# Optimization experiments

Hardware: AMD Instinct MI355X
Metric: run time of the kernel (lower is better)

The kernel has to match this reference:

```python
import jax, jax.numpy as jnp
import numpy as np

T, B, I, H, C, O = 4096, 8, 256, 512, 1024, 512
SCHEDULE = 1.0
UPPER_T = 0.3
NIND = int((1.0 - SCHEDULE) * (C - 2) * UPPER_T) + 1  # = 1 (argmax WTA)


def setup_inputs() -> dict:
    key = jax.random.key(0)
    ks = jax.random.split(key, 8)
    def lin(k, fan_out, fan_in):
        s = 1.0 / np.sqrt(fan_in)
        kw, kb = jax.random.split(k)
        return (jax.random.uniform(kw, (fan_out, fan_in), jnp.float32, -s, s),
                jax.random.uniform(kb, (fan_out,), jnp.float32, -s, s))
    i2m_w, i2m_b = lin(ks[0], H, I)
    m2h_w, m2h_b = lin(ks[1], C, H)
    h2o_w, h2o_b = lin(ks[2], O, C)
    return {
        "x": jax.random.normal(ks[3], (T, B, I), jnp.float32),
        "hidden1": jnp.zeros((1,), jnp.float32),  # unused dummy (overwritten in torch forward)
        "i2m_w": i2m_w, "i2m_b": i2m_b,
        "m2h_w": m2h_w, "m2h_b": m2h_b,
        "h2o_w": h2o_w, "h2o_b": h2o_b,
    }


def reference(x, hidden1, i2m_w, i2m_b, m2h_w, m2h_b, h2o_w, h2o_b):
    # linear -> relu
    h = jax.nn.relu(jnp.einsum('tbi,hi->tbh', x, i2m_w) + i2m_b)
    # linear -> relu -> concept pre-activations [T,B,C]
    c = jax.nn.relu(jnp.einsum('tbh,ch->tbc', h, m2h_w) + m2h_b)
    # winner-take-all: top-Nind scatter mask (replaces CPU argsort round-trip)
    _, idx = jax.lax.top_k(c, NIND)  # [T,B,NIND]
    t_ix = jnp.arange(c.shape[0])[:, None, None]
    b_ix = jnp.arange(c.shape[1])[None, :, None]
    mask = jnp.zeros_like(c).at[t_ix, b_ix, idx].set(1.0)
    m = c * mask
    # L2 normalize over concept axis
    m = m / jnp.linalg.norm(m, axis=-1, keepdims=True)
    out = jnp.einsum('tbc,oc->tbo', m, h2o_w) + h2o_b
    return jax.nn.log_softmax(out, axis=-1)
```

## Files before the change

### kernel.cpp

```cpp
#include <hip/hip_runtime.h>
#include <stdint.h>

#define M_ROWS 32768
#define I_DIM 256
#define H_DIM 512
#define C_DIM 1024
#define O_DIM 512

typedef __attribute__((ext_vector_type(8))) short bf16x8;
typedef __attribute__((ext_vector_type(4))) float f32x4;

__device__ __forceinline__ ushort bf16_rne(float f) {
    unsigned u = __float_as_uint(f);
    unsigned r = u + 0x7FFFu + ((u >> 16) & 1u);
    return (ushort)(r >> 16);
}
__device__ __forceinline__ float bf16_f32(ushort h) {
    return __uint_as_float(((unsigned)h) << 16);
}
__device__ __forceinline__ void split2(float f, ushort& hi, ushort& mid) {
    hi = bf16_rne(f);
    mid = bf16_rne(f - bf16_f32(hi));
}

__device__ __forceinline__ void async_ld16(const void* g, void* l) {
    __builtin_amdgcn_global_load_lds(
        (const __attribute__((address_space(1))) void*)g,
        (__attribute__((address_space(3))) void*)l, 16, 0, 0);
}

__device__ __forceinline__ unsigned long long packvi(float v, int col) {
    unsigned u = __float_as_uint(v);
    u = (u & 0x80000000u) ? ~u : (u | 0x80000000u);
    return ((unsigned long long)u << 32) | (unsigned)(~col);
}

__device__ __forceinline__ int slot_of(int kc, int row) {
    return (kc + ((row >> 1) & 3)) & 3;
}

__global__ __launch_bounds__(256)
void prep(const float* __restrict__ W1, ushort* __restrict__ w1h, ushort* __restrict__ w1m,
          const float* __restrict__ W2, ushort* __restrict__ w2h, ushort* __restrict__ w2m,
          const float* __restrict__ Wo, const float* __restrict__ bo,
          float* __restrict__ LS, unsigned long long* __restrict__ part) {
    __shared__ float sred[4];
    const int b = blockIdx.x;
    const int t = threadIdx.x;
    if (b < 320) {
        const int isW1 = (b < 64);
        const float* W = isW1 ? W1 : W2;
        ushort* hh = isW1 ? w1h : w2h;
        ushort* mm = isW1 ? w1m : w2m;
        const int K = isW1 ? I_DIM : H_DIM;
        const int cpr = K >> 3;
        int gid = (isW1 ? b : b - 64) * 256 + t;
        int row = gid / cpr;
        int rem = gid - row * cpr;
        int g = rem >> 2, kc = rem & 3;
        float4 v0 = *(const float4*)(W + (size_t)gid * 8);
        float4 v1 = *(const float4*)(W + (size_t)gid * 8 + 4);
        __align__(16) ushort h[8], m[8];
        float f[8];
        *(float4*)&f[0] = v0; *(float4*)&f[4] = v1;
        #pragma unroll
        for (int j = 0; j < 8; ++j) split2(f[j], h[j], m[j]);
        size_t dst = (size_t)row * K + g * 32 + slot_of(kc, row) * 8;
        *(uint4*)(hh + dst) = *(uint4*)h;
        *(uint4*)(mm + dst) = *(uint4*)m;
    } else if (b < 1344) {
        const int j = b - 320;
        float l0 = Wo[(size_t)t * C_DIM + j] + bo[t];
        float l1 = Wo[(size_t)(t + 256) * C_DIM + j] + bo[t + 256];

        float mx = fmaxf(l0, l1);
        #pragma unroll
        for (int off = 1; off < 64; off <<= 1)
            mx = fmaxf(mx, __shfl_xor(mx, off, 64));
        if ((t & 63) == 0) sred[t >> 6] = mx;
        __syncthreads();
        mx = fmaxf(fmaxf(sred[0], sred[1]), fmaxf(sred[2], sred[3]));
        __syncthreads();

        float s = expf(l0 - mx) + expf(l1 - mx);
        #pragma unroll
        for (int off = 1; off < 64; off <<= 1)
            s += __shfl_xor(s, off, 64);
        if ((t & 63) == 0) sred[t >> 6] = s;
        __syncthreads();
        s = sred[0] + sred[1] + sred[2] + sred[3];

        float lse = mx + logf(s);
        LS[(size_t)j * O_DIM + t] = l0 - lse;
        LS[(size_t)j * O_DIM + t + 256] = l1 - lse;
    } else {
        part[(b - 1344) * 256 + t] = 0ull;
    }
}

__global__ __launch_bounds__(256, 4)
void gemm1_mfma(const float* __restrict__ X, const ushort* __restrict__ W1h,
                const ushort* __restrict__ W1m, const float* __restrict__ b1,
                ushort* __restrict__ Hh, ushort* __restrict__ Hm) {
    __shared__ __align__(16) ushort LB[16384];
    ushort* As0 = LB;
    ushort* As1 = LB + 4096;
    ushort* Bs0 = LB + 8192;
    ushort* Bs1 = LB + 12288;

    const int tid = threadIdx.x;
    const int lane = tid & 63, wave = tid >> 6;
    const int wm = wave >> 1, wn = wave & 1;
    const int lcol = lane & 15, quad = lane >> 4;
    const int mBase = blockIdx.x * 128;
    const int nBase = blockIdx.y * 128;
    const int s_row = tid >> 1, s_half = tid & 1;
    const int bplane = wave >> 1;
    const ushort* wp = bplane ? W1m : W1h;
    const int brow0 = (wave & 1) * 64;
    const int lrow = lane >> 2, lk = (lane & 3) * 8;

    f32x4 acc[4][4];
    #pragma unroll
    for (int i = 0; i < 4; ++i)
        #pragma unroll
        for (int j = 0; j < 4; ++j)
            acc[i][j] = (f32x4){0.f, 0.f, 0.f, 0.f};

    int aoff[4], boff[4];
    #pragma unroll
    for (int t = 0; t < 4; ++t) {
        int ra = wm * 64 + t * 16 + lcol;
        int rb = wn * 64 + t * 16 + lcol;
        aoff[t] = ra * 32 + slot_of(quad, ra) * 8;
        boff[t] = rb * 32 + slot_of(quad, rb) * 8;
    }
    const int sl0 = slot_of(s_half * 2,     s_row);
    const int sl1 = slot_of(s_half * 2 + 1, s_row);

    for (int ks = 0; ks < I_DIM / 32; ++ks) {
        const int k0 = ks * 32;
        const float* ap = X + (size_t)(mBase + s_row) * I_DIM + k0 + s_half * 16;
        float4 f0 = ((const float4*)ap)[0];
        float4 f1 = ((const float4*)ap)[1];
        float4 f2 = ((const float4*)ap)[2];
        float4 f3 = ((const float4*)ap)[3];

        __syncthreads();

        #pragma unroll
        for (int i = 0; i < 4; ++i) {
            int r = brow0 + i * 16;
            const ushort* g = wp + (size_t)(nBase + r + lrow) * I_DIM + k0 + lk;
            async_ld16(g, (bplane ? Bs1 : Bs0) + r * 32);
        }

        float f[16];
        *(float4*)&f[0] = f0; *(float4*)&f[4] = f1;
        *(float4*)&f[8] = f2; *(float4*)&f[12] = f3;
        bf16x8 h0, h1, m0, m1;
        #pragma unroll
        for (int j = 0; j < 8; ++j) {
            ushort hu, mu;
            split2(f[j], hu, mu);
            h0[j] = (short)hu; m0[j] = (short)mu;
            split2(f[j + 8], hu, mu);
            h1[j] = (short)hu; m1[j] = (short)mu;
        }
        *(bf16x8*)&As0[s_row * 32 + sl0 * 8] = h0;
        *(bf16x8*)&As0[s_row * 32 + sl1 * 8] = h1;
        *(bf16x8*)&As1[s_row * 32 + sl0 * 8] = m0;
        *(bf16x8*)&As1[s_row * 32 + sl1 * 8] = m1;

        __syncthreads();

        bf16x8 af[4][2];
        #pragma unroll
        for (int mt = 0; mt < 4; ++mt) {
            af[mt][0] = *(const bf16x8*)&As0[aoff[mt]];
            af[mt][1] = *(const bf16x8*)&As1[aoff[mt]];
        }
        #pragma unroll
        for (int nt = 0; nt < 4; ++nt) {
            bf16x8 bh = *(const bf16x8*)&Bs0[boff[nt]];
            bf16x8 bm = *(const bf16x8*)&Bs1[boff[nt]];
            #pragma unroll
            for (int mt = 0; mt < 4; ++mt) {
                f32x4 a = acc[mt][nt];
                a = __builtin_amdgcn_mfma_f32_16x16x32_bf16(af[mt][1], bh, a, 0, 0, 0);
                a = __builtin_amdgcn_mfma_f32_16x16x32_bf16(af[mt][0], bm, a, 0, 0, 0);
                a = __builtin_amdgcn_mfma_f32_16x16x32_bf16(af[mt][0], bh, a, 0, 0, 0);
                acc[mt][nt] = a;
            }
        }
    }

    #pragma unroll
    for (int plane = 0; plane < 2; ++plane) {
        __syncthreads();
        #pragma unroll
        for (int nt = 0; nt < 4; ++nt) {
            int colRel = wn * 64 + nt * 16 + lcol;
            int g = colRel >> 5, kc = (colRel >> 3) & 3, pos = colRel & 7;
            float bias = b1[nBase + colRel];
            #pragma unroll
            for (int mt = 0; mt < 4; ++mt) {
                #pragma unroll
                for (int r = 0; r < 4; ++r) {
                    int rowRel = wm * 64 + mt * 16 + quad * 4 + r;
                    float v = fmaxf(acc[mt][nt][r] + bias, 0.f);
                    ushort hu, mu;
                    split2(v, hu, mu);
                    LB[rowRel * 128 + g * 32 + slot_of(kc, rowRel) * 8 + pos]
                        = plane ? mu : hu;
                }
            }
        }
        __syncthreads();
        ushort* dstp = plane ? Hm : Hh;
        #pragma unroll
        for (int l = 0; l < 8; ++l) {
            int c = l * 256 + tid;
            int row = c >> 4, idx = c & 15;
            *(uint4*)(dstp + (size_t)(mBase + row) * H_DIM + nBase + idx * 8)
                = *(const uint4*)&LB[row * 128 + idx * 8];
        }
    }
}

__global__ __launch_bounds__(256, 4)
void gemm2_mfma(const ushort* __restrict__ Hh, const ushort* __restrict__ Hm,
                const ushort* __restrict__ W2h, const ushort* __restrict__ W2m,
                const float* __restrict__ b2,
                unsigned long long* __restrict__ part) {
    __shared__ __align__(16) ushort As[2][128 * 32];
    __shared__ __align__(16) ushort Bs[2][128 * 32];
    const int tid = threadIdx.x;
    const int lane = tid & 63, wave = tid >> 6;
    const int wm = wave >> 1, wn = wave & 1;
    const int lcol = lane & 15, quad = lane >> 4;
    const int mBase = blockIdx.x * 128;
    const int nBase = blockIdx.y * 128;
    const int lrow = lane >> 2, lk = (lane & 3) * 8;

    const ushort* gsrc;
    ushort* lbase;
    switch (wave) {
        case 0: gsrc = Hh  + (size_t)mBase * H_DIM; lbase = As[0]; break;
        case 1: gsrc = Hm  + (size_t)mBase * H_DIM; lbase = As[1]; break;
        case 2: gsrc = W2h + (size_t)nBase * H_DIM; lbase = Bs[0]; break;
        default: gsrc = W2m + (size_t)nBase * H_DIM; lbase = Bs[1]; break;
    }

    f32x4 acc[4][4];
    #pragma unroll
    for (int i = 0; i < 4; ++i)
        #pragma unroll
        for (int j = 0; j < 4; ++j)
            acc[i][j] = (f32x4){0.f, 0.f, 0.f, 0.f};

    int aoff[4], boff[4];
    #pragma unroll
    for (int t = 0; t < 4; ++t) {
        int ra = wm * 64 + t * 16 + lcol;
        int rb = wn * 64 + t * 16 + lcol;
        aoff[t] = ra * 32 + slot_of(quad, ra) * 8;
        boff[t] = rb * 32 + slot_of(quad, rb) * 8;
    }

    for (int ks = 0; ks < H_DIM / 32; ++ks) {
        const int k0 = ks * 32;
        __syncthreads();
        #pragma unroll
        for (int j = 0; j < 8; ++j) {
            const ushort* g = gsrc + (size_t)(j * 16 + lrow) * H_DIM + k0 + lk;
            async_ld16(g, lbase + j * 512);
        }
        __syncthreads();

        bf16x8 af[4][2];
        #pragma unroll
        for (int mt = 0; mt < 4; ++mt) {
            af[mt][0] = *(const bf16x8*)&As[0][aoff[mt]];
            af[mt][1] = *(const bf16x8*)&As[1][aoff[mt]];
        }
        #pragma unroll
        for (int nt = 0; nt < 4; ++nt) {
            bf16x8 bh = *(const bf16x8*)&Bs[0][boff[nt]];
            bf16x8 bm = *(const bf16x8*)&Bs[1][boff[nt]];
            #pragma unroll
            for (int mt = 0; mt < 4; ++mt) {
                f32x4 a = acc[mt][nt];
                a = __builtin_amdgcn_mfma_f32_16x16x32_bf16(af[mt][1], bh, a, 0, 0, 0);
                a = __builtin_amdgcn_mfma_f32_16x16x32_bf16(af[mt][0], bm, a, 0, 0, 0);
                a = __builtin_amdgcn_mfma_f32_16x16x32_bf16(af[mt][0], bh, a, 0, 0, 0);
                acc[mt][nt] = a;
            }
        }
    }

    #pragma unroll
    for (int mt = 0; mt < 4; ++mt) {
        #pragma unroll
        for (int r = 0; r < 4; ++r) {
            unsigned long long best = 0ull;
            #pragma unroll
            for (int nt = 0; nt < 4; ++nt) {
                int col = nBase + wn * 64 + nt * 16 + lcol;
                float v = acc[mt][nt][r] + b2[col];
                unsigned long long p = packvi(v, col);
                if (p > best) best = p;
            }
            #pragma unroll
            for (int off = 1; off < 16; off <<= 1) {
                unsigned long long o = __shfl_xor((long long)best, off, 64);
                if (o > best) best = o;
            }
            if (lcol == 0) {
                int row = mBase + wm * 64 + mt * 16 + quad * 4 + r;
                atomicMax(&part[row], best);
            }
        }
    }
}

__global__ __launch_bounds__(256)
void gather_out(const unsigned long long* __restrict__ part,
                const float* __restrict__ LS, float* __restrict__ out) {
    const int tid = threadIdx.x;
    const int row = blockIdx.x * 2 + (tid >> 7);
    const int q = tid & 127;
    unsigned long long best = part[row];
    unsigned u = (unsigned)(best >> 32);
    float v = (u & 0x80000000u) ? __uint_as_float(u ^ 0x80000000u)
                                : __uint_as_float(~u);
    int col = (int)(~(unsigned)best) & (C_DIM - 1);
    int j = (v > 0.f) ? col : 0;
    float4 val = ((const float4*)LS)[(size_t)j * 128 + q];
    ((float4*)out)[(size_t)row * 128 + q] = val;
}

extern "C" void kernel_launch(void* const* d_in, const int* in_sizes, int n_in,
                              void* d_out, int out_size, void* d_ws, size_t ws_size,
                              hipStream_t stream) {
    const float* x     = (const float*)d_in[0];
    const float* i2m_w = (const float*)d_in[2];
    const float* i2m_b = (const float*)d_in[3];
    const float* m2h_w = (const float*)d_in[4];
    const float* m2h_b = (const float*)d_in[5];
    const float* h2o_w = (const float*)d_in[6];
    const float* h2o_b = (const float*)d_in[7];
    float* out = (float*)d_out;

    char* ws = (char*)d_ws;
    ushort* w1h = (ushort*)(ws);
    ushort* w1m = (ushort*)(ws + 262144);
    ushort* w2h = (ushort*)(ws + 524288);
    ushort* w2m = (ushort*)(ws + 1572864);
    float*  LS  = (float*)(ws + 2621440);
    unsigned long long* part = (unsigned long long*)(ws + 4718592);

    ushort* Hh = (ushort*)d_out;
    ushort* Hm = Hh + (size_t)M_ROWS * H_DIM;

    prep<<<1472, 256, 0, stream>>>(i2m_w, w1h, w1m, m2h_w, w2h, w2m,
                                   h2o_w, h2o_b, LS, part);
    gemm1_mfma<<<dim3(M_ROWS / 128, H_DIM / 128), 256, 0, stream>>>(
        x, w1h, w1m, i2m_b, Hh, Hm);
    gemm2_mfma<<<dim3(M_ROWS / 128, C_DIM / 128), 256, 0, stream>>>(
        Hh, Hm, w2h, w2m, m2h_b, part);
    gather_out<<<M_ROWS / 2, 256, 0, stream>>>(part, LS, out);
}
```

Baseline: 258.8 us.

## Double-buffer LDS staging in both GEMMs with tile swizzle and MFMA priority

Both GEMM kernels now use two LDS buffers. The next K-slice's global loads (async for the weights and H, register-staged for X) are issued before the current slice's MFMAs, and each iteration drops to a single barrier. Block indices are remapped so that neighbouring blocks share M/N tiles, for better L2 reuse. s_setprio raises wave priority around the MFMA section. The price is double the LDS footprint, with launch bounds lowered to 2 blocks per CU, which reduces occupancy.

```diff
diff --git a/kernel.cpp b/kernel.cpp
--- a/kernel.cpp
+++ b/kernel.cpp
@@ -98,22 +98,22 @@
     }
 }
 
-__global__ __launch_bounds__(256, 4)
+__global__ __launch_bounds__(256, 2)
 void gemm1_mfma(const float* __restrict__ X, const ushort* __restrict__ W1h,
                 const ushort* __restrict__ W1m, const float* __restrict__ b1,
                 ushort* __restrict__ Hh, ushort* __restrict__ Hm) {
-    __shared__ __align__(16) ushort LB[16384];
-    ushort* As0 = LB;
-    ushort* As1 = LB + 4096;
-    ushort* Bs0 = LB + 8192;
-    ushort* Bs1 = LB + 12288;
+    __shared__ __align__(16) ushort As[2][2][4096];
+    __shared__ __align__(16) ushort Bs[2][2][4096];
 
     const int tid = threadIdx.x;
     const int lane = tid & 63, wave = tid >> 6;
     const int wm = wave >> 1, wn = wave & 1;
     const int lcol = lane & 15, quad = lane >> 4;
-    const int mBase = blockIdx.x * 128;
-    const int nBase = blockIdx.y * 128;
+    const int d = blockIdx.x + (blockIdx.y << 8);
+    const int mT = ((d & 7) << 5) + ((d >> 3) >> 2);
+    const int nT = (d >> 3) & 3;
+    const int mBase = mT * 128;
+    const int nBase = nT * 128;
     const int s_row = tid >> 1, s_half = tid & 1;
     const int bplane = wave >> 1;
     const ushort* wp = bplane ? W1m : W1h;
@@ -135,29 +135,26 @@
         aoff[t] = ra * 32 + slot_of(quad, ra) * 8;
         boff[t] = rb * 32 + slot_of(quad, rb) * 8;
     }
-    const int sl0 = slot_of(s_half * 2,     s_row);
-    const int sl1 = slot_of(s_half * 2 + 1, s_row);
-
-    for (int ks = 0; ks < I_DIM / 32; ++ks) {
-        const int k0 = ks * 32;
-        const float* ap = X + (size_t)(mBase + s_row) * I_DIM + k0 + s_half * 16;
-        float4 f0 = ((const float4*)ap)[0];
-        float4 f1 = ((const float4*)ap)[1];
-        float4 f2 = ((const float4*)ap)[2];
-        float4 f3 = ((const float4*)ap)[3];
-
-        __syncthreads();
-
+    const int awr0 = s_row * 32 + slot_of(s_half * 2,     s_row) * 8;
+    const int awr1 = s_row * 32 + slot_of(s_half * 2 + 1, s_row) * 8;
+    const float* xrow = X + (size_t)(mBase + s_row) * I_DIM + s_half * 16;
+
+    auto loadX = [&](float* f, int k0) {
+        const float* ap = xrow + k0;
+        *(float4*)&f[0]  = ((const float4*)ap)[0];
+        *(float4*)&f[4]  = ((const float4*)ap)[1];
+        *(float4*)&f[8]  = ((const float4*)ap)[2];
+        *(float4*)&f[12] = ((const float4*)ap)[3];
+    };
+    auto stageB = [&](int buf, int k0) {
         #pragma unroll
         for (int i = 0; i < 4; ++i) {
             int r = brow0 + i * 16;
-            const ushort* g = wp + (size_t)(nBase + r + lrow) * I_DIM + k0 + lk;
-            async_ld16(g, (bplane ? Bs1 : Bs0) + r * 32);
-        }
-
-        float f[16];
-        *(float4*)&f[0] = f0; *(float4*)&f[4] = f1;
-        *(float4*)&f[8] = f2; *(float4*)&f[12] = f3;
+            async_ld16(wp + (size_t)(nBase + r + lrow) * I_DIM + k0 + lk,
+                       &Bs[buf][bplane][r * 32]);
+        }
+    };
+    auto writeA = [&](int buf, const float* f) {
         bf16x8 h0, h1, m0, m1;
         #pragma unroll
         for (int j = 0; j < 8; ++j) {
@@ -167,23 +164,41 @@
             split2(f[j + 8], hu, mu);
             h1[j] = (short)hu; m1[j] = (short)mu;
         }
-        *(bf16x8*)&As0[s_row * 32 + sl0 * 8] = h0;
-        *(bf16x8*)&As0[s_row * 32 + sl1 * 8] = h1;
-        *(bf16x8*)&As1[s_row * 32 + sl0 * 8] = m0;
-        *(bf16x8*)&As1[s_row * 32 + sl1 * 8] = m1;
-
-        __syncthreads();
+        *(bf16x8*)&As[buf][0][awr0] = h0;
+        *(bf16x8*)&As[buf][0][awr1] = h1;
+        *(bf16x8*)&As[buf][1][awr0] = m0;
+        *(bf16x8*)&As[buf][1][awr1] = m1;
+    };
+
+    {
+        float fx[16];
+        loadX(fx, 0);
+        stageB(0, 0);
+        writeA(0, fx);
+    }
+    __syncthreads();
+
+    const int NK = I_DIM / 32;
+    #pragma unroll 2
+    for (int ks = 0; ks < NK; ++ks) {
+        const int cur = ks & 1;
+        float fn[16];
+        if (ks + 1 < NK) {
+            loadX(fn, (ks + 1) * 32);
+            stageB(cur ^ 1, (ks + 1) * 32);
+        }
 
         bf16x8 af[4][2];
         #pragma unroll
         for (int mt = 0; mt < 4; ++mt) {
-            af[mt][0] = *(const bf16x8*)&As0[aoff[mt]];
-            af[mt][1] = *(const bf16x8*)&As1[aoff[mt]];
-        }
+            af[mt][0] = *(const bf16x8*)&As[cur][0][aoff[mt]];
+            af[mt][1] = *(const bf16x8*)&As[cur][1][aoff[mt]];
+        }
+        __builtin_amdgcn_s_setprio(1);
         #pragma unroll
         for (int nt = 0; nt < 4; ++nt) {
-            bf16x8 bh = *(const bf16x8*)&Bs0[boff[nt]];
-            bf16x8 bm = *(const bf16x8*)&Bs1[boff[nt]];
+            bf16x8 bh = *(const bf16x8*)&Bs[cur][0][boff[nt]];
+            bf16x8 bm = *(const bf16x8*)&Bs[cur][1][boff[nt]];
             #pragma unroll
             for (int mt = 0; mt < 4; ++mt) {
                 f32x4 a = acc[mt][nt];
@@ -193,8 +208,13 @@
                 acc[mt][nt] = a;
             }
         }
-    }
-
+        __builtin_amdgcn_s_setprio(0);
+
+        if (ks + 1 < NK) writeA(cur ^ 1, fn);
+        __syncthreads();
+    }
+
+    ushort* LB = &As[0][0][0];
     #pragma unroll
     for (int plane = 0; plane < 2; ++plane) {
         __syncthreads();
@@ -228,28 +248,32 @@
     }
 }
 
-__global__ __launch_bounds__(256, 4)
+__global__ __launch_bounds__(256, 2)
 void gemm2_mfma(const ushort* __restrict__ Hh, const ushort* __restrict__ Hm,
                 const ushort* __restrict__ W2h, const ushort* __restrict__ W2m,
                 const float* __restrict__ b2,
                 unsigned long long* __restrict__ part) {
-    __shared__ __align__(16) ushort As[2][128 * 32];
-    __shared__ __align__(16) ushort Bs[2][128 * 32];
+    __shared__ __align__(16) ushort As[2][2][4096];
+    __shared__ __align__(16) ushort Bs[2][2][4096];
     const int tid = threadIdx.x;
     const int lane = tid & 63, wave = tid >> 6;
     const int wm = wave >> 1, wn = wave & 1;
     const int lcol = lane & 15, quad = lane >> 4;
-    const int mBase = blockIdx.x * 128;
-    const int nBase = blockIdx.y * 128;
+    const int d = blockIdx.x + (blockIdx.y << 8);
+    const int mT = ((d & 7) << 5) + (d >> 6);
+    const int nT = (d >> 3) & 7;
+    const int mBase = mT * 128;
+    const int nBase = nT * 128;
     const int lrow = lane >> 2, lk = (lane & 3) * 8;
 
     const ushort* gsrc;
-    ushort* lbase;
+    ushort* lds0;
+    ushort* lds1;
     switch (wave) {
-        case 0: gsrc = Hh  + (size_t)mBase * H_DIM; lbase = As[0]; break;
-        case 1: gsrc = Hm  + (size_t)mBase * H_DIM; lbase = As[1]; break;
-        case 2: gsrc = W2h + (size_t)nBase * H_DIM; lbase = Bs[0]; break;
-        default: gsrc = W2m + (size_t)nBase * H_DIM; lbase = Bs[1]; break;
+        case 0:  gsrc = Hh  + (size_t)mBase * H_DIM; lds0 = As[0][0]; lds1 = As[1][0]; break;
+        case 1:  gsrc = Hm  + (size_t)mBase * H_DIM; lds0 = As[0][1]; lds1 = As[1][1]; break;
+        case 2:  gsrc = W2h + (size_t)nBase * H_DIM; lds0 = Bs[0][0]; lds1 = Bs[1][0]; break;
+        default: gsrc = W2m + (size_t)nBase * H_DIM; lds0 = Bs[0][1]; lds1 = Bs[1][1]; break;
     }
 
     f32x4 acc[4][4];
@@ -268,26 +292,33 @@
         boff[t] = rb * 32 + slot_of(quad, rb) * 8;
     }
 
-    for (int ks = 0; ks < H_DIM / 32; ++ks) {
-        const int k0 = ks * 32;
-        __syncthreads();
-        #pragma unroll
-        for (int j = 0; j < 8; ++j) {
-            const ushort* g = gsrc + (size_t)(j * 16 + lrow) * H_DIM + k0 + lk;
-            async_ld16(g, lbase + j * 512);
-        }
-        __syncthreads();
+    auto stage = [&](ushort* lb, int k0) {
+        #pragma unroll
+        for (int j = 0; j < 8; ++j)
+            async_ld16(gsrc + (size_t)(j * 16 + lrow) * H_DIM + k0 + lk,
+                       lb + j * 512);
+    };
+
+    stage(lds0, 0);
+    __syncthreads();
+
+    const int NK = H_DIM / 32;
+    #pragma unroll 2
+    for (int ks = 0; ks < NK; ++ks) {
+        const int cur = ks & 1;
+        if (ks + 1 < NK) stage(cur ? lds0 : lds1, (ks + 1) * 32);
 
         bf16x8 af[4][2];
         #pragma unroll
         for (int mt = 0; mt < 4; ++mt) {
-            af[mt][0] = *(const bf16x8*)&As[0][aoff[mt]];
-            af[mt][1] = *(const bf16x8*)&As[1][aoff[mt]];
-        }
+            af[mt][0] = *(const bf16x8*)&As[cur][0][aoff[mt]];
+            af[mt][1] = *(const bf16x8*)&As[cur][1][aoff[mt]];
+        }
+        __builtin_amdgcn_s_setprio(1);
         #pragma unroll
         for (int nt = 0; nt < 4; ++nt) {
-            bf16x8 bh = *(const bf16x8*)&Bs[0][boff[nt]];
-            bf16x8 bm = *(const bf16x8*)&Bs[1][boff[nt]];
+            bf16x8 bh = *(const bf16x8*)&Bs[cur][0][boff[nt]];
+            bf16x8 bm = *(const bf16x8*)&Bs[cur][1][boff[nt]];
             #pragma unroll
             for (int mt = 0; mt < 4; ++mt) {
                 f32x4 a = acc[mt][nt];
@@ -297,6 +328,8 @@
                 acc[mt][nt] = a;
             }
         }
+        __builtin_amdgcn_s_setprio(0);
+        __syncthreads();
     }
 
     #pragma unroll
```

Result: slower. 278.5 us (+7.6%).

## Enlarge gemm2 tiles to 256x256 with double-buffered LDS and swizzled block order

Applied to the files above, without the earlier changes.

Gemm2 now uses 256x256 output tiles computed by 512-thread blocks (8 waves in a 2x4 grid), so each wave holds an 8x4 fragment grid and each loaded tile is reused across more MFMAs. The K loop double-buffers LDS, issuing the next slice's async loads before computing on the current one and needing only one barrier per step. MFMA sections are raised with setprio, bias loads are hoisted out of the epilogue, and blocks are remapped in a grouped order for L2 locality. The cost is much higher register and LDS use per block (128 accumulator floats per thread), which lowers occupancy and risks spills.

```diff
diff --git a/kernel.cpp b/kernel.cpp
--- a/kernel.cpp
+++ b/kernel.cpp
@@ -228,86 +228,129 @@
     }
 }
 
-__global__ __launch_bounds__(256, 4)
+__global__ __launch_bounds__(512, 2)
 void gemm2_mfma(const ushort* __restrict__ Hh, const ushort* __restrict__ Hm,
                 const ushort* __restrict__ W2h, const ushort* __restrict__ W2m,
                 const float* __restrict__ b2,
                 unsigned long long* __restrict__ part) {
-    __shared__ __align__(16) ushort As[2][128 * 32];
-    __shared__ __align__(16) ushort Bs[2][128 * 32];
+    __shared__ __align__(16) ushort As[2][2][8192];
+    __shared__ __align__(16) ushort Bs[2][2][8192];
     const int tid = threadIdx.x;
     const int lane = tid & 63, wave = tid >> 6;
-    const int wm = wave >> 1, wn = wave & 1;
+    const int wm = wave >> 2, wn = wave & 3;
     const int lcol = lane & 15, quad = lane >> 4;
-    const int mBase = blockIdx.x * 128;
-    const int nBase = blockIdx.y * 128;
     const int lrow = lane >> 2, lk = (lane & 3) * 8;
 
+    const int d = blockIdx.x;
+    const int l = d >> 3;
+    const int mT = ((d & 7) << 4) + (l >> 2);
+    const int nT = l & 3;
+    const int mBase = mT * 256;
+    const int nBase = nT * 256;
+
+    const int m_id = wave >> 1;
+    const int shalf = wave & 1;
     const ushort* gsrc;
-    ushort* lbase;
-    switch (wave) {
-        case 0: gsrc = Hh  + (size_t)mBase * H_DIM; lbase = As[0]; break;
-        case 1: gsrc = Hm  + (size_t)mBase * H_DIM; lbase = As[1]; break;
-        case 2: gsrc = W2h + (size_t)nBase * H_DIM; lbase = Bs[0]; break;
-        default: gsrc = W2m + (size_t)nBase * H_DIM; lbase = Bs[1]; break;
-    }
-
-    f32x4 acc[4][4];
-    #pragma unroll
-    for (int i = 0; i < 4; ++i)
+    ushort* l0;
+    ushort* l1;
+    switch (m_id) {
+        case 0:  gsrc = Hh  + (size_t)mBase * H_DIM; l0 = &As[0][0][0]; l1 = &As[1][0][0]; break;
+        case 1:  gsrc = Hm  + (size_t)mBase * H_DIM; l0 = &As[0][1][0]; l1 = &As[1][1][0]; break;
+        case 2:  gsrc = W2h + (size_t)nBase * H_DIM; l0 = &Bs[0][0][0]; l1 = &Bs[1][0][0]; break;
+        default: gsrc = W2m + (size_t)nBase * H_DIM; l0 = &Bs[0][1][0]; l1 = &Bs[1][1][0]; break;
+    }
+    l0 += shalf * 4096;
+    l1 += shalf * 4096;
+    const ushort* gks = gsrc + (size_t)(shalf * 128 + lrow) * H_DIM + lk;
+
+    f32x4 acc[8][4];
+    #pragma unroll
+    for (int i = 0; i < 8; ++i)
         #pragma unroll
         for (int j = 0; j < 4; ++j)
             acc[i][j] = (f32x4){0.f, 0.f, 0.f, 0.f};
 
-    int aoff[4], boff[4];
+    int aoff[8], boff[4];
+    #pragma unroll
+    for (int t = 0; t < 8; ++t) {
+        int ra = wm * 128 + t * 16 + lcol;
+        aoff[t] = ra * 32 + slot_of(quad, ra) * 8;
+    }
     #pragma unroll
     for (int t = 0; t < 4; ++t) {
-        int ra = wm * 64 + t * 16 + lcol;
         int rb = wn * 64 + t * 16 + lcol;
-        aoff[t] = ra * 32 + slot_of(quad, ra) * 8;
         boff[t] = rb * 32 + slot_of(quad, rb) * 8;
     }
 
-    for (int ks = 0; ks < H_DIM / 32; ++ks) {
-        const int k0 = ks * 32;
-        __syncthreads();
-        #pragma unroll
-        for (int j = 0; j < 8; ++j) {
-            const ushort* g = gsrc + (size_t)(j * 16 + lrow) * H_DIM + k0 + lk;
-            async_ld16(g, lbase + j * 512);
-        }
-        __syncthreads();
-
-        bf16x8 af[4][2];
-        #pragma unroll
-        for (int mt = 0; mt < 4; ++mt) {
-            af[mt][0] = *(const bf16x8*)&As[0][aoff[mt]];
-            af[mt][1] = *(const bf16x8*)&As[1][aoff[mt]];
-        }
+    auto stage = [&](ushort* lb, int k0) {
+        #pragma unroll
+        for (int j = 0; j < 8; ++j)
+            async_ld16(gks + k0 + (size_t)(j * 16) * H_DIM, lb + j * 512);
+    };
+
+    stage(l0, 0);
+    asm volatile("s_waitcnt vmcnt(0)" ::: "memory");
+    __builtin_amdgcn_s_barrier();
+    __builtin_amdgcn_sched_barrier(0);
+
+    const int NK = H_DIM / 32;
+    #pragma unroll 2
+    for (int ks = 0; ks < NK; ++ks) {
+        const int cur = ks & 1;
+        if (ks < NK - 1) {
+            stage(cur ? l0 : l1, (ks + 1) * 32);
+            __builtin_amdgcn_sched_barrier(0);
+        }
+
+        bf16x8 bh[4], bm[4];
         #pragma unroll
         for (int nt = 0; nt < 4; ++nt) {
-            bf16x8 bh = *(const bf16x8*)&Bs[0][boff[nt]];
-            bf16x8 bm = *(const bf16x8*)&Bs[1][boff[nt]];
+            bh[nt] = *(const bf16x8*)&Bs[cur][0][boff[nt]];
+            bm[nt] = *(const bf16x8*)&Bs[cur][1][boff[nt]];
+        }
+        #pragma unroll
+        for (int half = 0; half < 2; ++half) {
+            bf16x8 ah[4], am[4];
             #pragma unroll
             for (int mt = 0; mt < 4; ++mt) {
-                f32x4 a = acc[mt][nt];
-                a = __builtin_amdgcn_mfma_f32_16x16x32_bf16(af[mt][1], bh, a, 0, 0, 0);
-                a = __builtin_amdgcn_mfma_f32_16x16x32_bf16(af[mt][0], bm, a, 0, 0, 0);
-                a = __builtin_amdgcn_mfma_f32_16x16x32_bf16(af[mt][0], bh, a, 0, 0, 0);
-                acc[mt][nt] = a;
-            }
-        }
-    }
-
-    #pragma unroll
-    for (int mt = 0; mt < 4; ++mt) {
+                ah[mt] = *(const bf16x8*)&As[cur][0][aoff[half * 4 + mt]];
+                am[mt] = *(const bf16x8*)&As[cur][1][aoff[half * 4 + mt]];
+            }
+            __builtin_amdgcn_s_setprio(1);
+            #pragma unroll
+            for (int nt = 0; nt < 4; ++nt) {
+                #pragma unroll
+                for (int mt = 0; mt < 4; ++mt) {
+                    f32x4 a = acc[half * 4 + mt][nt];
+                    a = __builtin_amdgcn_mfma_f32_16x16x32_bf16(am[mt], bh[nt], a, 0, 0, 0);
+                    a = __builtin_amdgcn_mfma_f32_16x16x32_bf16(ah[mt], bm[nt], a, 0, 0, 0);
+                    a = __builtin_amdgcn_mfma_f32_16x16x32_bf16(ah[mt], bh[nt], a, 0, 0, 0);
+                    acc[half * 4 + mt][nt] = a;
+                }
+            }
+            __builtin_amdgcn_s_setprio(0);
+        }
+
+        if (ks < NK - 1)
+            asm volatile("s_waitcnt vmcnt(0)" ::: "memory");
+        __builtin_amdgcn_s_barrier();
+        __builtin_amdgcn_sched_barrier(0);
+    }
+
+    float bias[4];
+    #pragma unroll
+    for (int nt = 0; nt < 4; ++nt)
+        bias[nt] = b2[nBase + wn * 64 + nt * 16 + lcol];
+
+    #pragma unroll
+    for (int mt = 0; mt < 8; ++mt) {
         #pragma unroll
         for (int r = 0; r < 4; ++r) {
             unsigned long long best = 0ull;
             #pragma unroll
             for (int nt = 0; nt < 4; ++nt) {
                 int col = nBase + wn * 64 + nt * 16 + lcol;
-                float v = acc[mt][nt][r] + b2[col];
+                float v = acc[mt][nt][r] + bias[nt];
                 unsigned long long p = packvi(v, col);
                 if (p > best) best = p;
             }
@@ -317,7 +360,7 @@
                 if (o > best) best = o;
             }
             if (lcol == 0) {
-                int row = mBase + wm * 64 + mt * 16 + quad * 4 + r;
+                int row = mBase + wm * 128 + mt * 16 + quad * 4 + r;
                 atomicMax(&part[row], best);
             }
         }
@@ -367,7 +410,7 @@
                                    h2o_w, h2o_b, LS, part);
     gemm1_mfma<<<dim3(M_ROWS / 128, H_DIM / 128), 256, 0, stream>>>(
         x, w1h, w1m, i2m_b, Hh, Hm);
-    gemm2_mfma<<<dim3(M_ROWS / 128, C_DIM / 128), 256, 0, stream>>>(
+    gemm2_mfma<<<(M_ROWS / 256) * (C_DIM / 256), 512, 0, stream>>>(
         Hh, Hm, w2h, w2m, m2h_b, part);
     gather_out<<<M_ROWS / 2, 256, 0, stream>>>(part, LS, out);
 }
```

New measurement: 244.5 us. 1.06x faster.
